# Performance work log

Hardware: AMD Instinct MI355X
Metric: run time of the kernel (lower is better)

Reference implementation:

```python
import jax, jax.numpy as jnp
import numpy as np

ALPHA = 1.0
BETA = 1.0


def setup_inputs() -> dict:
    key = jax.random.key(0)
    k1, k2, k3, k4 = jax.random.split(key, 4)
    B_, S, D_in, D_out, R = 4, 64, 8192, 8192, 16
    x = jax.random.normal(k1, (B_, S, D_in), dtype=jnp.float32)
    original_weight = jax.random.normal(k2, (D_out, D_in), dtype=jnp.float32) * 0.02
    A = jax.random.normal(k3, (D_out, R), dtype=jnp.float32) * 0.02
    Bm = jax.random.normal(k4, (R, D_in), dtype=jnp.float32) * 0.02
    return {"x": x, "original_weight": original_weight, "A": A, "B": Bm}


def reference(x, original_weight, A, B):
    # delta_weight = alpha * (A @ B)  -> [D_out, D_in]
    delta_weight = ALPHA * jnp.matmul(A, B)
    # F.linear(x, W + beta*delta) = x @ (W + beta*delta)^T
    W = original_weight + BETA * delta_weight
    return jnp.einsum("bsd,od->bso", x, W)
```

## Files before the change

### kernel.cpp

```cpp
#include <hip/hip_runtime.h>
#include <stdint.h>


#define DM 256
#define DK 8192
#define DN 8192
#define RLORA 16

#define TN 64
#define BK 128
#define KSPLIT 4
#define KCHUNK (DK / KSPLIT)
#define NITER (KCHUNK / BK)

typedef short bf16x8 __attribute__((ext_vector_type(8)));
typedef float f32x4v __attribute__((ext_vector_type(4)));

__device__ __forceinline__ unsigned short f2bf(float f) {
  unsigned u = __builtin_bit_cast(unsigned, f);
  u += 0x7FFFu + ((u >> 16) & 1u);
  return (unsigned short)(u >> 16);
}

__device__ __forceinline__ bf16x8 pack8(float4 a, float4 b) {
  bf16x8 r;
  r[0] = (short)f2bf(a.x); r[1] = (short)f2bf(a.y);
  r[2] = (short)f2bf(a.z); r[3] = (short)f2bf(a.w);
  r[4] = (short)f2bf(b.x); r[5] = (short)f2bf(b.y);
  r[6] = (short)f2bf(b.z); r[7] = (short)f2bf(b.w);
  return r;
}

__global__ __launch_bounds__(256) void prep_x(
    const float* __restrict__ x, const float* __restrict__ Bm,
    unsigned short* __restrict__ xb, float* __restrict__ y32) {
  const int ks = blockIdx.x;
  const int m0 = blockIdx.y * 4;
  const int t = threadIdx.x;
  const int k = ks * 1024 + t * 4;
  const int K64 = k >> 6, s = (k >> 5) & 1, oct = (k >> 3) & 3;
  const int e = k & 7;
  float4 xv[4];
#pragma unroll
  for (int i = 0; i < 4; ++i) {
    const int m = m0 + i;
    const int g = m >> 4, r = m & 15;
    xv[i] = *(const float4*)(x + (size_t)m * DK + k);
    ushort4 h;
    h.x = f2bf(xv[i].x); h.y = f2bf(xv[i].y);
    h.z = f2bf(xv[i].z); h.w = f2bf(xv[i].w);
    const size_t chunk = (size_t)(K64 * 32 + s * 16 + g) * 64 + oct * 16 + r;
    *(ushort4*)(xb + chunk * 8 + e) = h;
  }
  float acc[4][RLORA];
#pragma unroll
  for (int r = 0; r < RLORA; ++r) {
    float4 b = *(const float4*)(Bm + (size_t)r * DK + k);
#pragma unroll
    for (int i = 0; i < 4; ++i)
      acc[i][r] = xv[i].x * b.x + xv[i].y * b.y + xv[i].z * b.z + xv[i].w * b.w;
  }
#pragma unroll
  for (int off = 32; off >= 1; off >>= 1)
#pragma unroll
    for (int i = 0; i < 4; ++i)
#pragma unroll
      for (int r = 0; r < RLORA; ++r)
        acc[i][r] += __shfl_xor(acc[i][r], off, 64);
  __shared__ float red[4][4][RLORA];
  const int lane = t & 63, wv = t >> 6;
  if (lane == 0) {
#pragma unroll
    for (int i = 0; i < 4; ++i)
#pragma unroll
      for (int r = 0; r < RLORA; ++r) red[wv][i][r] = acc[i][r];
  }
  __syncthreads();
  if (t < 64) {
    int i = t >> 4, r = t & 15;
    float sum = red[0][i][r] + red[1][i][r] + red[2][i][r] + red[3][i][r];
    atomicAdd(y32 + (m0 + i) * RLORA + r, sum);
  }
}

__global__ __launch_bounds__(512, 4) void lora_gemm(
    const unsigned short* __restrict__ xb,
    const float* __restrict__ W,
    const float* __restrict__ y32,
    const float* __restrict__ Aw,
    float* __restrict__ out,
    float* __restrict__ part) {
  __shared__ unsigned short wsm[2][8192];

  const int tid = threadIdx.x;
  const int lane = tid & 63, w = tid >> 6;
  const int qr = lane & 15, quad = lane >> 4;

  const int bid = blockIdx.x;
  const int xcd = bid & 7;
  const int kz = xcd >> 1;
  const int nblk = (bid >> 3) + ((xcd & 1) << 6);
  const int n0 = nblk * TN;
  const int kb = kz * KCHUNK;

  const int f0 = w * 2, f1 = f0 + 1;
  const float* wsrc0 = W + (size_t)(n0 + (f0 & 3) * 16 + qr) * DK + kb +
                       (f0 >> 2) * 32 + quad * 8;
  const float* wsrc1 = W + (size_t)(n0 + (f1 & 3) * 16 + qr) * DK + kb +
                       (f1 >> 2) * 32 + quad * 8;
  const unsigned wdst0 = (unsigned)(f0 * 64 + lane) * 16;
  const unsigned wdst1 = wdst0 + 1024;

  const bf16x8* ap = (const bf16x8*)xb + ((size_t)(kz * 32) * 32) * 64 + lane;

  f32x4v acc[2][4];
#pragma unroll
  for (int a = 0; a < 2; ++a)
#pragma unroll
    for (int b = 0; b < 4; ++b) acc[a][b] = (f32x4v){0.f, 0.f, 0.f, 0.f};

  float4 g[2][4];
  g[0][0] = *(const float4*)(wsrc0);
  g[0][1] = *(const float4*)(wsrc0 + 4);
  g[0][2] = *(const float4*)(wsrc1);
  g[0][3] = *(const float4*)(wsrc1 + 4);
  g[1][0] = *(const float4*)(wsrc0 + BK);
  g[1][1] = *(const float4*)(wsrc0 + BK + 4);
  g[1][2] = *(const float4*)(wsrc1 + BK);
  g[1][3] = *(const float4*)(wsrc1 + BK + 4);
  *(bf16x8*)((char*)wsm[0] + wdst0) = pack8(g[0][0], g[0][1]);
  *(bf16x8*)((char*)wsm[0] + wdst1) = pack8(g[0][2], g[0][3]);
  __syncthreads();

#pragma unroll 2
  for (int it = 0; it < NITER; ++it) {
    const char* wcur = (const char*)wsm[it & 1];
    bf16x8 av[2][2];
#pragma unroll
    for (int si = 0; si < 2; ++si)
#pragma unroll
      for (int mt = 0; mt < 2; ++mt)
        av[si][mt] =
            ap[(size_t)((it * 2) * 32 + si * 16 + w * 2 + mt) * 64];
#pragma unroll
    for (int s = 0; s < 2; ++s) {
      bf16x8 b[4];
#pragma unroll
      for (int sub = 0; sub < 4; ++sub)
        b[sub] = *(const bf16x8*)(wcur + (((s * 4 + sub) * 64 + lane) * 16));
#pragma unroll
      for (int mt = 0; mt < 2; ++mt)
#pragma unroll
        for (int sub = 0; sub < 4; ++sub)
          acc[mt][sub] = __builtin_amdgcn_mfma_f32_16x16x32_bf16(
              av[s][mt], b[sub], acc[mt][sub], 0, 0, 0);
    }
#pragma unroll
    for (int si = 0; si < 2; ++si)
#pragma unroll
      for (int mt = 0; mt < 2; ++mt)
        av[si][mt] =
            ap[(size_t)((it * 2 + 1) * 32 + si * 16 + w * 2 + mt) * 64];
    if (it + 2 < NITER) {
      const float* p0 = wsrc0 + (size_t)(it + 2) * BK;
      const float* p1 = wsrc1 + (size_t)(it + 2) * BK;
      g[it & 1][0] = *(const float4*)(p0);
      g[it & 1][1] = *(const float4*)(p0 + 4);
      g[it & 1][2] = *(const float4*)(p1);
      g[it & 1][3] = *(const float4*)(p1 + 4);
    }
#pragma unroll
    for (int s = 2; s < 4; ++s) {
      bf16x8 b[4];
#pragma unroll
      for (int sub = 0; sub < 4; ++sub)
        b[sub] = *(const bf16x8*)(wcur + (((s * 4 + sub) * 64 + lane) * 16));
#pragma unroll
      for (int mt = 0; mt < 2; ++mt)
#pragma unroll
        for (int sub = 0; sub < 4; ++sub)
          acc[mt][sub] = __builtin_amdgcn_mfma_f32_16x16x32_bf16(
              av[s - 2][mt], b[sub], acc[mt][sub], 0, 0, 0);
    }
    if (it + 1 < NITER) {
      char* wnxt = (char*)wsm[(it + 1) & 1];
      *(bf16x8*)(wnxt + wdst0) = pack8(g[(it + 1) & 1][0], g[(it + 1) & 1][1]);
      *(bf16x8*)(wnxt + wdst1) = pack8(g[(it + 1) & 1][2], g[(it + 1) & 1][3]);
    }
    __syncthreads();
  }

  if (kz == 0) {
    const float4 z = {0.f, 0.f, 0.f, 0.f};
    bf16x8 b[4];
#pragma unroll
    for (int sub = 0; sub < 4; ++sub) {
      const float* ap2 = Aw + (size_t)(n0 + sub * 16 + qr) * RLORA + quad * 8;
      float4 p0 = (quad < 2) ? *(const float4*)(ap2) : z;
      float4 p1 = (quad < 2) ? *(const float4*)(ap2 + 4) : z;
      b[sub] = pack8(p0, p1);
    }
#pragma unroll
    for (int mt = 0; mt < 2; ++mt) {
      const float* yp = y32 + (size_t)(w * 32 + mt * 16 + qr) * RLORA + quad * 8;
      float4 q0 = (quad < 2) ? *(const float4*)(yp) : z;
      float4 q1 = (quad < 2) ? *(const float4*)(yp + 4) : z;
      bf16x8 avt = pack8(q0, q1);
#pragma unroll
      for (int sub = 0; sub < 4; ++sub)
        acc[mt][sub] = __builtin_amdgcn_mfma_f32_16x16x32_bf16(
            avt, b[sub], acc[mt][sub], 0, 0, 0);
    }
  }

  if (part) {
    float* pb = part + (size_t)kz * DM * DN;
#pragma unroll
    for (int mt = 0; mt < 2; ++mt)
#pragma unroll
      for (int sub = 0; sub < 4; ++sub) {
        float* p = pb + (size_t)(w * 32 + mt * 16 + quad * 4) * DN +
                   n0 + sub * 16 + qr;
#pragma unroll
        for (int rg = 0; rg < 4; ++rg) p[(size_t)rg * DN] = acc[mt][sub][rg];
      }
  } else {
    float* ob = out;
#pragma unroll
    for (int mt = 0; mt < 2; ++mt)
#pragma unroll
      for (int sub = 0; sub < 4; ++sub) {
        float* p = ob + (size_t)(w * 32 + mt * 16 + quad * 4) * DN +
                   n0 + sub * 16 + qr;
#pragma unroll
        for (int rg = 0; rg < 4; ++rg)
          atomicAdd(p + (size_t)rg * DN, acc[mt][sub][rg]);
      }
  }
}

__global__ __launch_bounds__(256) void reduce_k(
    const float* __restrict__ part, float* __restrict__ out) {
  size_t i = ((size_t)blockIdx.x * 256 + threadIdx.x) * 4;
  float4 s = *(const float4*)(part + i);
#pragma unroll
  for (int kzi = 1; kzi < KSPLIT; ++kzi) {
    float4 v = *(const float4*)(part + (size_t)kzi * DM * DN + i);
    s.x += v.x; s.y += v.y; s.z += v.z; s.w += v.w;
  }
  *(float4*)(out + i) = s;
}

extern "C" void kernel_launch(void* const* d_in, const int* in_sizes, int n_in,
                              void* d_out, int out_size, void* d_ws, size_t ws_size,
                              hipStream_t stream) {
  const float* x  = (const float*)d_in[0];
  const float* W  = (const float*)d_in[1];
  const float* A  = (const float*)d_in[2];
  const float* Bm = (const float*)d_in[3];
  float* out = (float*)d_out;

  unsigned short* xb = (unsigned short*)d_ws;
  float* y32 = (float*)((char*)d_ws + (4u << 20));
  size_t base_bytes = (4u << 20) + 16384;
  size_t part_bytes = (size_t)KSPLIT * DM * DN * 4;
  bool use_part = ws_size >= base_bytes + part_bytes;
  float* part = use_part ? (float*)((char*)d_ws + base_bytes) : nullptr;

  if (!use_part)
    hipMemsetAsync(d_out, 0, (size_t)out_size * sizeof(float), stream);
  hipMemsetAsync(y32, 0, (size_t)DM * RLORA * sizeof(float), stream);
  prep_x<<<dim3(8, 64), 256, 0, stream>>>(x, Bm, xb, y32);
  lora_gemm<<<512, 512, 0, stream>>>(xb, W, y32, A, out, part);
  if (use_part) reduce_k<<<2048, 256, 0, stream>>>(part, out);
}
```

Measured before the change: 422.0 us.

## Fuse split-K reduction into GEMM via last-arriver counters; transpose-reduce LoRA projection

Drops the separate reduce_k kernel. Each GEMM block now bumps a per-N-tile atomic counter after writing its partial, and the last of the KSPLIT blocks sums all four partials into the output. This saves a kernel launch and lets the reduction overlap with other blocks still computing, at the cost of an extra fence, a barrier and the serial tail work done by the last block. Separately, prep_x swaps its wave-shuffle butterfly reduction for an LDS transpose with per-thread sums, which needs a 64KB shared buffer and may reduce occupancy.

```diff
diff --git a/kernel.cpp b/kernel.cpp
--- a/kernel.cpp
+++ b/kernel.cpp
@@ -60,26 +60,27 @@
     for (int i = 0; i < 4; ++i)
       acc[i][r] = xv[i].x * b.x + xv[i].y * b.y + xv[i].z * b.z + xv[i].w * b.w;
   }
-#pragma unroll
-  for (int off = 32; off >= 1; off >>= 1)
-#pragma unroll
-    for (int i = 0; i < 4; ++i)
-#pragma unroll
-      for (int r = 0; r < RLORA; ++r)
-        acc[i][r] += __shfl_xor(acc[i][r], off, 64);
-  __shared__ float red[4][4][RLORA];
-  const int lane = t & 63, wv = t >> 6;
-  if (lane == 0) {
-#pragma unroll
-    for (int i = 0; i < 4; ++i)
-#pragma unroll
-      for (int r = 0; r < RLORA; ++r) red[wv][i][r] = acc[i][r];
-  }
+  __shared__ float tr[256][64];
+#pragma unroll
+  for (int i = 0; i < 4; ++i)
+#pragma unroll
+    for (int r = 0; r < RLORA; ++r) {
+      const int v = i * 16 + r;
+      tr[t][(v + t) & 63] = acc[i][r];
+    }
+  __syncthreads();
+  const int v = t & 63, q = t >> 6;
+  float sq = 0.f;
+#pragma unroll
+  for (int j = 0; j < 64; ++j)
+    sq += tr[q * 64 + j][(v + j) & 63];
+  __syncthreads();
+  ((float*)tr)[q * 64 + v] = sq;
   __syncthreads();
   if (t < 64) {
-    int i = t >> 4, r = t & 15;
-    float sum = red[0][i][r] + red[1][i][r] + red[2][i][r] + red[3][i][r];
-    atomicAdd(y32 + (m0 + i) * RLORA + r, sum);
+    float sum = ((float*)tr)[t] + ((float*)tr)[64 + t] +
+                ((float*)tr)[128 + t] + ((float*)tr)[192 + t];
+    atomicAdd(y32 + (m0 + (t >> 4)) * RLORA + (t & 15), sum);
   }
 }
 
@@ -89,8 +90,10 @@
     const float* __restrict__ y32,
     const float* __restrict__ Aw,
     float* __restrict__ out,
-    float* __restrict__ part) {
+    float* __restrict__ part,
+    int* __restrict__ cnt) {
   __shared__ unsigned short wsm[2][8192];
+  __shared__ int red_old;
 
   const int tid = threadIdx.x;
   const int lane = tid & 63, w = tid >> 6;
@@ -224,6 +227,30 @@
 #pragma unroll
         for (int rg = 0; rg < 4; ++rg) p[(size_t)rg * DN] = acc[mt][sub][rg];
       }
+    __threadfence();
+    __syncthreads();
+    if (tid == 0)
+      red_old = __hip_atomic_fetch_add(&cnt[nblk], 1, __ATOMIC_ACQ_REL,
+                                       __HIP_MEMORY_SCOPE_AGENT);
+    __syncthreads();
+    if (red_old == KSPLIT - 1) {
+      __threadfence();
+#pragma unroll
+      for (int c = 0; c < 8; ++c) {
+        const int fidx = c * 512 + tid;
+        const int row = fidx >> 4, col4 = fidx & 15;
+        const size_t ad = (size_t)row * DN + n0 + col4 * 4;
+        float4 s0 = *(const float4*)(part + ad);
+        const float4 s1 = *(const float4*)(part + (size_t)1 * DM * DN + ad);
+        const float4 s2 = *(const float4*)(part + (size_t)2 * DM * DN + ad);
+        const float4 s3 = *(const float4*)(part + (size_t)3 * DM * DN + ad);
+        s0.x += s1.x + s2.x + s3.x;
+        s0.y += s1.y + s2.y + s3.y;
+        s0.z += s1.z + s2.z + s3.z;
+        s0.w += s1.w + s2.w + s3.w;
+        *(float4*)(out + ad) = s0;
+      }
+    }
   } else {
     float* ob = out;
 #pragma unroll
@@ -237,18 +264,6 @@
           atomicAdd(p + (size_t)rg * DN, acc[mt][sub][rg]);
       }
   }
-}
-
-__global__ __launch_bounds__(256) void reduce_k(
-    const float* __restrict__ part, float* __restrict__ out) {
-  size_t i = ((size_t)blockIdx.x * 256 + threadIdx.x) * 4;
-  float4 s = *(const float4*)(part + i);
-#pragma unroll
-  for (int kzi = 1; kzi < KSPLIT; ++kzi) {
-    float4 v = *(const float4*)(part + (size_t)kzi * DM * DN + i);
-    s.x += v.x; s.y += v.y; s.z += v.z; s.w += v.w;
-  }
-  *(float4*)(out + i) = s;
 }
 
 extern "C" void kernel_launch(void* const* d_in, const int* in_sizes, int n_in,
@@ -262,15 +277,15 @@
 
   unsigned short* xb = (unsigned short*)d_ws;
   float* y32 = (float*)((char*)d_ws + (4u << 20));
-  size_t base_bytes = (4u << 20) + 16384;
+  int* cnt = (int*)((char*)y32 + 16384);
+  size_t base_bytes = (4u << 20) + 16384 + 512;
   size_t part_bytes = (size_t)KSPLIT * DM * DN * 4;
   bool use_part = ws_size >= base_bytes + part_bytes;
   float* part = use_part ? (float*)((char*)d_ws + base_bytes) : nullptr;
 
   if (!use_part)
     hipMemsetAsync(d_out, 0, (size_t)out_size * sizeof(float), stream);
-  hipMemsetAsync(y32, 0, (size_t)DM * RLORA * sizeof(float), stream);
+  hipMemsetAsync(y32, 0, DM * RLORA * sizeof(float) + 512, stream);
   prep_x<<<dim3(8, 64), 256, 0, stream>>>(x, Bm, xb, y32);
-  lora_gemm<<<512, 512, 0, stream>>>(xb, W, y32, A, out, part);
-  if (use_part) reduce_k<<<2048, 256, 0, stream>>>(part, out);
-}
+  lora_gemm<<<512, 512, 0, stream>>>(xb, W, y32, A, out, part, cnt);
+}
```

Result: slower. 637.1 us (+51.0%).

## Replace shuffle reduction and atomics in prep_x with LDS transpose and partial buffers

Applied to the files above, without the earlier changes.

The per-block reduction of x·B^T partials now goes through a shared-memory transpose with rotated indexing instead of a 6-step shuffle tree over 64 values. Each k-slice writes its partial sums to a separate buffer slot rather than using atomicAdd. The GEMM kernel then sums the 8 slices when it forms the LoRA operand. This also removes the memset of the y32 buffer. In exchange it uses 64KB of LDS per prep block and adds 8x the loads for the small y operand in the GEMM epilogue.

```diff
diff --git a/kernel.cpp b/kernel.cpp
--- a/kernel.cpp
+++ b/kernel.cpp
@@ -33,7 +33,7 @@
 
 __global__ __launch_bounds__(256) void prep_x(
     const float* __restrict__ x, const float* __restrict__ Bm,
-    unsigned short* __restrict__ xb, float* __restrict__ y32) {
+    unsigned short* __restrict__ xb, float* __restrict__ y32p) {
   const int ks = blockIdx.x;
   const int m0 = blockIdx.y * 4;
   const int t = threadIdx.x;
@@ -60,33 +60,34 @@
     for (int i = 0; i < 4; ++i)
       acc[i][r] = xv[i].x * b.x + xv[i].y * b.y + xv[i].z * b.z + xv[i].w * b.w;
   }
-#pragma unroll
-  for (int off = 32; off >= 1; off >>= 1)
-#pragma unroll
-    for (int i = 0; i < 4; ++i)
-#pragma unroll
-      for (int r = 0; r < RLORA; ++r)
-        acc[i][r] += __shfl_xor(acc[i][r], off, 64);
-  __shared__ float red[4][4][RLORA];
-  const int lane = t & 63, wv = t >> 6;
-  if (lane == 0) {
-#pragma unroll
-    for (int i = 0; i < 4; ++i)
-#pragma unroll
-      for (int r = 0; r < RLORA; ++r) red[wv][i][r] = acc[i][r];
-  }
+  __shared__ float tr[256][64];
+#pragma unroll
+  for (int i = 0; i < 4; ++i)
+#pragma unroll
+    for (int r = 0; r < RLORA; ++r) {
+      const int v = i * 16 + r;
+      tr[t][(v + t) & 63] = acc[i][r];
+    }
+  __syncthreads();
+  const int v = t & 63, q = t >> 6;
+  float sq = 0.f;
+#pragma unroll
+  for (int j = 0; j < 64; ++j)
+    sq += tr[q * 64 + j][(v + j) & 63];
+  __syncthreads();
+  ((float*)tr)[q * 64 + v] = sq;
   __syncthreads();
   if (t < 64) {
-    int i = t >> 4, r = t & 15;
-    float sum = red[0][i][r] + red[1][i][r] + red[2][i][r] + red[3][i][r];
-    atomicAdd(y32 + (m0 + i) * RLORA + r, sum);
+    float sum = ((float*)tr)[t] + ((float*)tr)[64 + t] +
+                ((float*)tr)[128 + t] + ((float*)tr)[192 + t];
+    y32p[(size_t)ks * (DM * RLORA) + (m0 + (t >> 4)) * RLORA + (t & 15)] = sum;
   }
 }
 
 __global__ __launch_bounds__(512, 4) void lora_gemm(
     const unsigned short* __restrict__ xb,
     const float* __restrict__ W,
-    const float* __restrict__ y32,
+    const float* __restrict__ y32p,
     const float* __restrict__ Aw,
     float* __restrict__ out,
     float* __restrict__ part) {
@@ -202,9 +203,19 @@
     }
 #pragma unroll
     for (int mt = 0; mt < 2; ++mt) {
-      const float* yp = y32 + (size_t)(w * 32 + mt * 16 + qr) * RLORA + quad * 8;
-      float4 q0 = (quad < 2) ? *(const float4*)(yp) : z;
-      float4 q1 = (quad < 2) ? *(const float4*)(yp + 4) : z;
+      float4 q0 = z, q1 = z;
+      if (quad < 2) {
+        const float* yp =
+            y32p + (size_t)(w * 32 + mt * 16 + qr) * RLORA + quad * 8;
+#pragma unroll
+        for (int ks = 0; ks < 8; ++ks) {
+          const float* sp = yp + (size_t)ks * (DM * RLORA);
+          const float4 a0 = *(const float4*)(sp);
+          const float4 a1 = *(const float4*)(sp + 4);
+          q0.x += a0.x; q0.y += a0.y; q0.z += a0.z; q0.w += a0.w;
+          q1.x += a1.x; q1.y += a1.y; q1.z += a1.z; q1.w += a1.w;
+        }
+      }
       bf16x8 avt = pack8(q0, q1);
 #pragma unroll
       for (int sub = 0; sub < 4; ++sub)
@@ -261,16 +272,15 @@
   float* out = (float*)d_out;
 
   unsigned short* xb = (unsigned short*)d_ws;
-  float* y32 = (float*)((char*)d_ws + (4u << 20));
-  size_t base_bytes = (4u << 20) + 16384;
+  float* y32p = (float*)((char*)d_ws + (4u << 20));
+  size_t base_bytes = (4u << 20) + (size_t)8 * DM * RLORA * 4;
   size_t part_bytes = (size_t)KSPLIT * DM * DN * 4;
   bool use_part = ws_size >= base_bytes + part_bytes;
   float* part = use_part ? (float*)((char*)d_ws + base_bytes) : nullptr;
 
   if (!use_part)
     hipMemsetAsync(d_out, 0, (size_t)out_size * sizeof(float), stream);
-  hipMemsetAsync(y32, 0, (size_t)DM * RLORA * sizeof(float), stream);
-  prep_x<<<dim3(8, 64), 256, 0, stream>>>(x, Bm, xb, y32);
-  lora_gemm<<<512, 512, 0, stream>>>(xb, W, y32, A, out, part);
+  prep_x<<<dim3(8, 64), 256, 0, stream>>>(x, Bm, xb, y32p);
+  lora_gemm<<<512, 512, 0, stream>>>(xb, W, y32p, A, out, part);
   if (use_part) reduce_k<<<2048, 256, 0, stream>>>(part, out);
 }
```

After: 422.7 us. Within noise of the previous version (+0.1%).
